# Kernel tuning notes

Measured on AMD Instinct MI355X. Metric: run time of the kernel, lower is better.

The kernel has to match this reference:

```python
import jax, jax.numpy as jnp
import numpy as np

B, S, H, F, E, K = 2, 2048, 1024, 4096, 8, 2


def setup_inputs() -> dict:
    key = jax.random.key(0)
    ks = jax.random.split(key, 5)
    scale = 0.02
    return {
        "hidden_states": jax.random.normal(ks[0], (B, S, H), jnp.float32),
        "gate_w": jax.random.normal(ks[1], (H, E), jnp.float32) * scale,  # nn.Linear(H,E,bias=False)
        "w1": jax.random.normal(ks[2], (E, H, F), jnp.float32) * scale,   # per-expert fc1
        "b1": jnp.zeros((E, F), jnp.float32),
        "w2": jax.random.normal(ks[3], (E, F, H), jnp.float32) * scale,   # per-expert fc2
        "b2": jnp.zeros((E, H), jnp.float32),
    }


def reference(hidden_states, gate_w, w1, b1, w2, b2):
    b, s, h = hidden_states.shape
    x = hidden_states.reshape(b * s, h)  # [T, H]
    T = x.shape[0]
    n_experts = gate_w.shape[1]

    # --- Top-K gating ---
    router_logits = x @ gate_w                      # [T, E]
    router_probs = jax.nn.softmax(router_logits, axis=-1)
    topk_probs, topk_idx = jax.lax.top_k(router_probs, K)  # [T, K]
    topk_probs = topk_probs / topk_probs.sum(axis=-1, keepdims=True)
    aux_loss = n_experts * jnp.sum(router_probs.mean(axis=0) ** 2)

    # --- Combine weights: scatter normalized top-k probs into dense [T, E] ---
    combine_w = jnp.zeros((T, n_experts), x.dtype).at[
        jnp.arange(T)[:, None], topk_idx
    ].add(topk_probs)

    # --- Expert MLPs (dense per-expert batched GEMM; zero combine weight drops unrouted) ---
    hidden = jax.nn.relu(jnp.einsum('th,ehf->etf', x, w1) + b1[:, None, :])  # [E, T, F]
    expert_out = jnp.einsum('etf,efh->eth', hidden, w2) + b2[:, None, :]     # [E, T, H]

    out = jnp.einsum('te,eth->th', combine_w, expert_out)  # weighted combine
    return out.reshape(b, s, h), aux_loss
```

## Files before the change

kernel.cpp:

```cpp
#include <hip/hip_runtime.h>
#include <hip/hip_bf16.h>
#include <cstdint>

#define AS1 __attribute__((address_space(1)))
#define AS3 __attribute__((address_space(3)))
#define SBAR() asm volatile("s_barrier" ::: "memory")

typedef __attribute__((ext_vector_type(8))) short short8x;
typedef __attribute__((ext_vector_type(4))) float f32x4;

static constexpr int T    = 4096;
static constexpr int HD   = 1024;
static constexpr int FD   = 4096;
static constexpr int NE   = 8;
static constexpr int P    = T * 2;
static constexpr int PPAD = P + 256;
static constexpr int MAXT256 = P / 256 + NE;
static constexpr int RTB  = 16;
static constexpr int RNB  = T / RTB;

struct TileDesc { int e; int start; int rows; int pad; };

__device__ __forceinline__ uint16_t f2bf(float f) {
  uint32_t u = __builtin_bit_cast(uint32_t, f);
  u += 0x7FFFu + ((u >> 16) & 1u);
  return (uint16_t)(u >> 16);
}
__device__ __forceinline__ float bf2f(uint16_t b) {
  uint32_t u = ((uint32_t)b) << 16;
  return __builtin_bit_cast(float, u);
}

__device__ __forceinline__ void gload_lds16(const void* g, void* l) {
  __builtin_amdgcn_global_load_lds((const AS1 uint32_t*)g, (AS3 uint32_t*)l, 16, 0, 0);
}

__device__ __forceinline__ short8x ds128(uint32_t addr) {
  short8x r;
  asm volatile("ds_read_b128 %0, %1" : "=v"(r) : "v"(addr));
  return r;
}

__global__ __launch_bounds__(256) void cvt_x_kernel(const float* __restrict__ x,
                                                    uint16_t* __restrict__ xb) {
  size_t i = ((size_t)blockIdx.x * 256 + threadIdx.x) * 4;
  float4 v = *(const float4*)&x[i];
  ushort4 o;
  o.x = f2bf(v.x); o.y = f2bf(v.y); o.z = f2bf(v.z); o.w = f2bf(v.w);
  *(ushort4*)&xb[i] = o;
}

__global__ __launch_bounds__(256) void transpose_cvt_kernel(
    const float* __restrict__ in, uint16_t* __restrict__ out, int R, int C) {
  __shared__ float tile[64][65];
  int z = blockIdx.z;
  const float* inp = in + (size_t)z * R * C;
  uint16_t* outp = out + (size_t)z * R * C;
  int r0 = blockIdx.y * 64, c0 = blockIdx.x * 64;
  int tid = threadIdx.x;
  int lr = tid >> 4;
  int lc4 = (tid & 15) * 4;
#pragma unroll
  for (int p = 0; p < 4; ++p) {
    float4 v = *(const float4*)&inp[(size_t)(r0 + lr + p * 16) * C + c0 + lc4];
    tile[lr + p * 16][lc4 + 0] = v.x;
    tile[lr + p * 16][lc4 + 1] = v.y;
    tile[lr + p * 16][lc4 + 2] = v.z;
    tile[lr + p * 16][lc4 + 3] = v.w;
  }
  __syncthreads();
#pragma unroll
  for (int p = 0; p < 4; ++p) {
    int c = lr + p * 16;
    ushort4 o;
    o.x = f2bf(tile[lc4 + 0][c]);
    o.y = f2bf(tile[lc4 + 1][c]);
    o.z = f2bf(tile[lc4 + 2][c]);
    o.w = f2bf(tile[lc4 + 3][c]);
    *(ushort4*)&outp[(size_t)(c0 + c) * R + r0 + lc4] = o;
  }
}

__global__ __launch_bounds__(256) void router_kernel(
    const float* __restrict__ x, const float* __restrict__ gate_w,
    int* __restrict__ topk_idx, float* __restrict__ topk_w,
    float* __restrict__ part_sums, int* __restrict__ part_counts) {
  __shared__ float g[NE * HD];
  __shared__ float ls[NE];
  __shared__ int   lc[NE];
  int tid = threadIdx.x;
  for (int i = tid; i < NE * HD; i += 256)
    g[(i & 7) * HD + (i >> 3)] = gate_w[i];
  if (tid < NE) { ls[tid] = 0.f; lc[tid] = 0; }
  __syncthreads();
  int wave = tid >> 6, lane = tid & 63;
  float psum[NE];
#pragma unroll
  for (int e = 0; e < NE; ++e) psum[e] = 0.f;

  for (int tt = 0; tt < RTB / 4; ++tt) {
    int t = blockIdx.x * RTB + wave * (RTB / 4) + tt;
    const float* xr = x + (size_t)t * HD;
    float acc[NE];
#pragma unroll
    for (int e = 0; e < NE; ++e) acc[e] = 0.f;
    for (int i = 0; i < HD / 64; ++i) {
      float xv = xr[lane + i * 64];
#pragma unroll
      for (int e = 0; e < NE; ++e) acc[e] += xv * g[e * HD + lane + i * 64];
    }
#pragma unroll
    for (int off = 32; off > 0; off >>= 1)
#pragma unroll
      for (int e = 0; e < NE; ++e) acc[e] += __shfl_down(acc[e], off);
    if (lane == 0) {
      float m = acc[0];
#pragma unroll
      for (int e = 1; e < NE; ++e) m = fmaxf(m, acc[e]);
      float p[NE], s = 0.f;
#pragma unroll
      for (int e = 0; e < NE; ++e) { p[e] = expf(acc[e] - m); s += p[e]; }
      float inv = 1.f / s;
#pragma unroll
      for (int e = 0; e < NE; ++e) { p[e] *= inv; psum[e] += p[e]; }
      int i0 = 0;
#pragma unroll
      for (int e = 1; e < NE; ++e) if (p[e] > p[i0]) i0 = e;
      int i1 = (i0 == 0) ? 1 : 0;
#pragma unroll
      for (int e = 0; e < NE; ++e) if (e != i0 && e != i1 && p[e] > p[i1]) i1 = e;
      float wsum = p[i0] + p[i1];
      topk_idx[t * 2] = i0; topk_idx[t * 2 + 1] = i1;
      topk_w[t * 2] = p[i0] / wsum; topk_w[t * 2 + 1] = p[i1] / wsum;
      atomicAdd(&lc[i0], 1); atomicAdd(&lc[i1], 1);
    }
  }
  if (lane == 0)
#pragma unroll
    for (int e = 0; e < NE; ++e) atomicAdd(&ls[e], psum[e]);
  __syncthreads();
  if (tid < NE) {
    part_sums[blockIdx.x * NE + tid]   = ls[tid];
    part_counts[blockIdx.x * NE + tid] = lc[tid];
  }
}

__global__ __launch_bounds__(64) void finalize_kernel(
    const int* __restrict__ part_counts, const float* __restrict__ part_sums,
    int* __restrict__ offsets, TileDesc* __restrict__ desc256,
    int* __restrict__ ntiles256, float* __restrict__ aux_out) {
  __shared__ int   csh[NE];
  __shared__ float ssh[NE];
  int tid = threadIdx.x;
  if (tid < NE) {
    int c = 0; float s = 0.f;
    for (int b = 0; b < RNB; ++b) {
      c += part_counts[b * NE + tid];
      s += part_sums[b * NE + tid];
    }
    csh[tid] = c; ssh[tid] = s;
  }
  __syncthreads();
  if (tid == 0) {
    int off = 0, nt2 = 0;
    for (int e = 0; e < NE; ++e) {
      offsets[e] = off;
      int c = csh[e];
      for (int i = 0; i < c; i += 256) {
        int rows = c - i; if (rows > 256) rows = 256;
        desc256[nt2].e = e; desc256[nt2].start = off + i; desc256[nt2].rows = rows;
        desc256[nt2].pad = 0; nt2++;
      }
      off += c;
    }
    *ntiles256 = nt2;
    float aux = 0.f;
    for (int e = 0; e < NE; ++e) {
      float mean = ssh[e] / (float)T;
      aux += mean * mean;
    }
    *aux_out = (float)NE * aux;
  }
}

__global__ __launch_bounds__(256) void scatter_kernel(
    const int* __restrict__ topk_idx, const int* __restrict__ offsets,
    int* __restrict__ fill, int* __restrict__ pair_tok, int* __restrict__ tok_pos) {
  int t = blockIdx.x * 256 + threadIdx.x;
  int lane = threadIdx.x & 63;
  unsigned long long below = (lane == 63) ? ~0ull >> 1
                                          : ((1ull << (lane + 1)) - 1) >> 1;
#pragma unroll
  for (int k = 0; k < 2; ++k) {
    int e = topk_idx[t * 2 + k];
    int pos = 0;
    for (int ex = 0; ex < NE; ++ex) {
      unsigned long long m = __ballot(e == ex);
      if (e == ex) {
        int leader = __ffsll((long long)m) - 1;
        int cnt = __popcll(m);
        int base = 0;
        if (lane == leader) base = atomicAdd(&fill[ex], cnt);
        base = __shfl(base, leader);
        pos = base + __popcll(m & below);
      }
    }
    int pp = offsets[e] + pos;
    pair_tok[pp] = t;
    tok_pos[t * 2 + k] = pp;
  }
}

template <int KD, int ND, bool GATHER, bool RELU>
__global__ __launch_bounds__(512, 2) void moe_gemm8(
    const uint16_t* __restrict__ A, const int* __restrict__ pair_tok,
    const uint16_t* __restrict__ Bw, const float* __restrict__ bias,
    uint16_t* __restrict__ C, const TileDesc* __restrict__ desc,
    const int* __restrict__ nt_ptr) {
  constexpr int NBC   = ND / 256;
  constexpr int NT    = KD / 64;
  constexpr int ASLOT = 16384;
  constexpr int BOFF  = 2 * ASLOT;
  constexpr int GRIDT = NBC * MAXT256;

  extern __shared__ char smem[];
  uint16_t* lds = (uint16_t*)smem;
  int* rowA = (int*)(smem + 131072);

  int orig = blockIdx.x;
  int work = (orig & 7) * (GRIDT / 8) + (orig >> 3);
  int nb = work % NBC;
  int mt = work / NBC;
  if (mt >= *nt_ptr) return;
  TileDesc d = desc[mt];

  int tid = threadIdx.x, lane = tid & 63, wave = tid >> 6;
  int wm = wave >> 2, wn = wave & 3;

  if constexpr (GATHER) {
    if (tid < 256) rowA[tid] = (tid < d.rows) ? pair_tok[d.start + tid] : 0;
    __syncthreads();
  }

  int wl8 = wave * 8 + (lane >> 3);
  int colel = (((lane & 7) ^ (lane >> 3)) << 3);
  const uint16_t* Asrc[4];
  const uint16_t* Bsrc[4];
#pragma unroll
  for (int i = 0; i < 4; ++i) {
    int r = i * 64 + wl8;
    int gr;
    if constexpr (GATHER) gr = rowA[r]; else gr = d.start + r;
    Asrc[i] = A + (size_t)gr * KD + colel;
    Bsrc[i] = Bw + ((size_t)d.e * ND + nb * 256 + r) * KD + colel;
  }

  auto stage = [&](int slot, int kt) {
    int ko = kt * 64;
#pragma unroll
    for (int i = 0; i < 4; ++i)
      gload_lds16(Asrc[i] + ko, &lds[slot * ASLOT + i * 4096 + wave * 512]);
#pragma unroll
    for (int j = 0; j < 4; ++j)
      gload_lds16(Bsrc[j] + ko, &lds[BOFF + slot * ASLOT + j * 4096 + wave * 512]);
  };

  uint32_t ldsu = (uint32_t)(uintptr_t)(AS3 char*)smem;
  int rd0 = (lane & 15) * 64 + ((((lane >> 4)) ^ (lane & 7)) << 3);
  int rd1 = (lane & 15) * 64 + ((((lane >> 4) | 4) ^ (lane & 7)) << 3);
  uint32_t aA0 = ldsu + (uint32_t)(wm * 8192 + rd0) * 2;
  uint32_t aA1 = ldsu + (uint32_t)(wm * 8192 + rd1) * 2;
  uint32_t aB0 = ldsu + (uint32_t)(BOFF + wn * 4096 + rd0) * 2;
  uint32_t aB1 = ldsu + (uint32_t)(BOFF + wn * 4096 + rd1) * 2;

  f32x4 acc[8][4];
#pragma unroll
  for (int i = 0; i < 8; ++i)
#pragma unroll
    for (int j = 0; j < 4; ++j) acc[i][j] = (f32x4){0.f, 0.f, 0.f, 0.f};

  short8x aq[4][2], bA[2][2], bB[2][2];

  stage(0, 0);
  stage(1, 1);
  asm volatile("s_waitcnt vmcnt(8)" ::: "memory");
  SBAR();

  for (int kt = 0; kt < NT; ++kt) {
    int slot = kt & 1;
    uint32_t sa = slot ? 32768u : 0u;

#pragma unroll
    for (int fm = 0; fm < 4; ++fm) {
      aq[fm][0] = ds128(aA0 + sa + fm * 2048);
      aq[fm][1] = ds128(aA1 + sa + fm * 2048);
    }
#pragma unroll
    for (int fn = 0; fn < 2; ++fn) {
      bA[fn][0] = ds128(aB0 + sa + fn * 2048);
      bA[fn][1] = ds128(aB1 + sa + fn * 2048);
    }
    SBAR();
    asm volatile("s_waitcnt lgkmcnt(0)" ::: "memory");
    __builtin_amdgcn_sched_barrier(0);
    __builtin_amdgcn_s_setprio(1);
#pragma unroll
    for (int fm = 0; fm < 4; ++fm)
#pragma unroll
      for (int fn = 0; fn < 2; ++fn) {
        acc[fm][fn] = __builtin_amdgcn_mfma_f32_16x16x32_bf16(aq[fm][0], bA[fn][0], acc[fm][fn], 0, 0, 0);
        acc[fm][fn] = __builtin_amdgcn_mfma_f32_16x16x32_bf16(aq[fm][1], bA[fn][1], acc[fm][fn], 0, 0, 0);
      }
    __builtin_amdgcn_s_setprio(0);
    SBAR();

#pragma unroll
    for (int fn = 0; fn < 2; ++fn) {
      bB[fn][0] = ds128(aB0 + sa + (fn + 2) * 2048);
      bB[fn][1] = ds128(aB1 + sa + (fn + 2) * 2048);
    }
    SBAR();
    asm volatile("s_waitcnt lgkmcnt(0)" ::: "memory");
    __builtin_amdgcn_sched_barrier(0);
    __builtin_amdgcn_s_setprio(1);
#pragma unroll
    for (int fm = 0; fm < 4; ++fm)
#pragma unroll
      for (int fn = 0; fn < 2; ++fn) {
        acc[fm][fn + 2] = __builtin_amdgcn_mfma_f32_16x16x32_bf16(aq[fm][0], bB[fn][0], acc[fm][fn + 2], 0, 0, 0);
        acc[fm][fn + 2] = __builtin_amdgcn_mfma_f32_16x16x32_bf16(aq[fm][1], bB[fn][1], acc[fm][fn + 2], 0, 0, 0);
      }
    __builtin_amdgcn_s_setprio(0);
    SBAR();

#pragma unroll
    for (int fm = 0; fm < 4; ++fm) {
      aq[fm][0] = ds128(aA0 + sa + 8192 + fm * 2048);
      aq[fm][1] = ds128(aA1 + sa + 8192 + fm * 2048);
    }
    SBAR();
    asm volatile("s_waitcnt lgkmcnt(0)" ::: "memory");
    __builtin_amdgcn_sched_barrier(0);
    __builtin_amdgcn_s_setprio(1);
#pragma unroll
    for (int fm = 0; fm < 4; ++fm)
#pragma unroll
      for (int fn = 0; fn < 2; ++fn) {
        acc[fm + 4][fn + 2] = __builtin_amdgcn_mfma_f32_16x16x32_bf16(aq[fm][0], bB[fn][0], acc[fm + 4][fn + 2], 0, 0, 0);
        acc[fm + 4][fn + 2] = __builtin_amdgcn_mfma_f32_16x16x32_bf16(aq[fm][1], bB[fn][1], acc[fm + 4][fn + 2], 0, 0, 0);
      }
    __builtin_amdgcn_s_setprio(0);
    SBAR();

    bool more = (kt + 2 < NT);
    if (more) stage(slot, kt + 2);
    __builtin_amdgcn_s_setprio(1);
#pragma unroll
    for (int fm = 0; fm < 4; ++fm)
#pragma unroll
      for (int fn = 0; fn < 2; ++fn) {
        acc[fm + 4][fn] = __builtin_amdgcn_mfma_f32_16x16x32_bf16(aq[fm][0], bA[fn][0], acc[fm + 4][fn], 0, 0, 0);
        acc[fm + 4][fn] = __builtin_amdgcn_mfma_f32_16x16x32_bf16(aq[fm][1], bA[fn][1], acc[fm + 4][fn], 0, 0, 0);
      }
    __builtin_amdgcn_s_setprio(0);
    if (more) asm volatile("s_waitcnt vmcnt(8)" ::: "memory");
    else      asm volatile("s_waitcnt vmcnt(0)" ::: "memory");
    SBAR();
  }

  int rq = (lane >> 4) * 4, cl = lane & 15;
  float bv[4];
#pragma unroll
  for (int fn = 0; fn < 4; ++fn)
    bv[fn] = bias[d.e * ND + nb * 256 + wn * 64 + fn * 16 + cl];
#pragma unroll
  for (int fm = 0; fm < 8; ++fm) {
    int rb = wm * 128 + fm * 16 + rq;
#pragma unroll
    for (int fn = 0; fn < 4; ++fn) {
      int col = nb * 256 + wn * 64 + fn * 16 + cl;
#pragma unroll
      for (int q = 0; q < 4; ++q) {
        int r = rb + q;
        if (r < d.rows) {
          float v = acc[fm][fn][q] + bv[fn];
          if constexpr (RELU) v = fmaxf(v, 0.f);
          C[(size_t)(d.start + r) * ND + col] = f2bf(v);
        }
      }
    }
  }
}

__global__ __launch_bounds__(256) void combine_kernel(
    const uint16_t* __restrict__ po, const int* __restrict__ tok_pos,
    const float* __restrict__ topk_w, float* __restrict__ out) {
  int t = blockIdx.x;
  int c = threadIdx.x * 4;
  int p0 = tok_pos[t * 2], p1 = tok_pos[t * 2 + 1];
  float w0 = topk_w[t * 2], w1 = topk_w[t * 2 + 1];
  ushort4 a = *(const ushort4*)&po[(size_t)p0 * HD + c];
  ushort4 b = *(const ushort4*)&po[(size_t)p1 * HD + c];
  float4 o;
  o.x = w0 * bf2f(a.x) + w1 * bf2f(b.x);
  o.y = w0 * bf2f(a.y) + w1 * bf2f(b.y);
  o.z = w0 * bf2f(a.z) + w1 * bf2f(b.z);
  o.w = w0 * bf2f(a.w) + w1 * bf2f(b.w);
  *(float4*)&out[(size_t)t * HD + c] = o;
}

extern "C" void kernel_launch(void* const* d_in, const int* in_sizes, int n_in,
                              void* d_out, int out_size, void* d_ws, size_t ws_size,
                              hipStream_t stream) {
  const float* x      = (const float*)d_in[0];
  const float* gate_w = (const float*)d_in[1];
  const float* w1     = (const float*)d_in[2];
  const float* b1     = (const float*)d_in[3];
  const float* w2     = (const float*)d_in[4];
  const float* b2     = (const float*)d_in[5];
  float* out = (float*)d_out;
  (void)in_sizes; (void)n_in; (void)out_size; (void)ws_size;

  char* w = (char*)d_ws;
  size_t off = 0;
  auto alloc = [&](size_t bytes) -> void* {
    void* p = w + off;
    off = (off + bytes + 255) & ~(size_t)255;
    return p;
  };
  int*      meta      = (int*)alloc(256);
  int*      fill      = meta;
  int*      offsets   = (int*)alloc(256);
  int*      ntiles256 = offsets + 8;
  TileDesc* desc256   = (TileDesc*)alloc(sizeof(TileDesc) * 64);
  int*      topk_idx  = (int*)alloc(sizeof(int) * P);
  float*    topk_w    = (float*)alloc(sizeof(float) * P);
  int*      tok_pos   = (int*)alloc(sizeof(int) * P);
  int*      pair_tok  = (int*)alloc(sizeof(int) * PPAD);
  float*    psums     = (float*)alloc(sizeof(float) * RNB * NE);
  int*      pcounts   = (int*)alloc(sizeof(int) * RNB * NE);
  uint16_t* xb        = (uint16_t*)alloc((size_t)T * HD * 2);
  uint16_t* w1t       = (uint16_t*)alloc((size_t)NE * FD * HD * 2);
  uint16_t* w2t       = (uint16_t*)alloc((size_t)NE * HD * FD * 2);
  uint16_t* hidden    = (uint16_t*)alloc((size_t)PPAD * FD * 2);
  uint16_t* pout      = (uint16_t*)alloc((size_t)PPAD * HD * 2);

  constexpr int GLDS = 131072 + 1024;

  hipMemsetAsync(meta, 0, 256, stream);
  cvt_x_kernel<<<(T * HD) / 1024, 256, 0, stream>>>(x, xb);
  transpose_cvt_kernel<<<dim3(FD / 64, HD / 64, NE), 256, 0, stream>>>(w1, w1t, HD, FD);
  transpose_cvt_kernel<<<dim3(HD / 64, FD / 64, NE), 256, 0, stream>>>(w2, w2t, FD, HD);
  router_kernel<<<RNB, 256, 0, stream>>>(x, gate_w, topk_idx, topk_w, psums, pcounts);
  finalize_kernel<<<1, 64, 0, stream>>>(pcounts, psums, offsets, desc256, ntiles256,
                                        out + (size_t)T * HD);
  scatter_kernel<<<T / 256, 256, 0, stream>>>(topk_idx, offsets, fill, pair_tok, tok_pos);
  moe_gemm8<HD, FD, true, true><<<(FD / 256) * MAXT256, 512, GLDS, stream>>>(
      xb, pair_tok, w1t, b1, hidden, desc256, ntiles256);
  moe_gemm8<FD, HD, false, false><<<(HD / 256) * MAXT256, 512, GLDS, stream>>>(
      hidden, nullptr, w2t, b2, pout, desc256, ntiles256);
  combine_kernel<<<T, 256, 0, stream>>>(pout, tok_pos, topk_w, out);
}
```

Before: 417.2 us.

## Use 128-row tiles for second expert GEMM and pipeline LDS reads with MFMAs

The second expert GEMM (K=4096, N=1024) now runs on 128-row M tiles with its own tile descriptor list, doubling the number of workgroups so more CUs are busy on the small-N GEMM. The grid remap now groups tiles so each of eight groups owns a contiguous set of M tiles across N blocks. The inner loop replaces the full lgkmcnt(0) waits and extra barriers with staged partial waits, so MFMAs start as soon as their operands arrive from LDS. Smaller tiles give less operand reuse per load, and the new wait counts have to match the issued reads exactly.

After: 412.1 us. About the same (-1.2%).

```diff
diff --git a/kernel.cpp b/kernel.cpp
--- a/kernel.cpp
+++ b/kernel.cpp
@@ -5,6 +5,8 @@
 #define AS1 __attribute__((address_space(1)))
 #define AS3 __attribute__((address_space(3)))
 #define SBAR() asm volatile("s_barrier" ::: "memory")
+#define LGKM_SB(n) do { asm volatile("s_waitcnt lgkmcnt(" #n ")" ::: "memory"); \
+                        __builtin_amdgcn_sched_barrier(0); } while (0)
 
 typedef __attribute__((ext_vector_type(8))) short short8x;
 typedef __attribute__((ext_vector_type(4))) float f32x4;
@@ -16,6 +18,7 @@
 static constexpr int P    = T * 2;
 static constexpr int PPAD = P + 256;
 static constexpr int MAXT256 = P / 256 + NE;
+static constexpr int MAXT128 = P / 128 + NE;
 static constexpr int RTB  = 16;
 static constexpr int RNB  = T / RTB;
 
@@ -30,11 +33,9 @@
   uint32_t u = ((uint32_t)b) << 16;
   return __builtin_bit_cast(float, u);
 }
-
 __device__ __forceinline__ void gload_lds16(const void* g, void* l) {
   __builtin_amdgcn_global_load_lds((const AS1 uint32_t*)g, (AS3 uint32_t*)l, 16, 0, 0);
 }
-
 __device__ __forceinline__ short8x ds128(uint32_t addr) {
   short8x r;
   asm volatile("ds_read_b128 %0, %1" : "=v"(r) : "v"(addr));
@@ -147,8 +148,8 @@
 
 __global__ __launch_bounds__(64) void finalize_kernel(
     const int* __restrict__ part_counts, const float* __restrict__ part_sums,
-    int* __restrict__ offsets, TileDesc* __restrict__ desc256,
-    int* __restrict__ ntiles256, float* __restrict__ aux_out) {
+    int* __restrict__ offsets, TileDesc* __restrict__ desc256, TileDesc* __restrict__ desc128,
+    int* __restrict__ ntiles256, int* __restrict__ ntiles128, float* __restrict__ aux_out) {
   __shared__ int   csh[NE];
   __shared__ float ssh[NE];
   int tid = threadIdx.x;
@@ -162,18 +163,24 @@
   }
   __syncthreads();
   if (tid == 0) {
-    int off = 0, nt2 = 0;
+    int off = 0, n2 = 0, n1 = 0;
     for (int e = 0; e < NE; ++e) {
       offsets[e] = off;
       int c = csh[e];
       for (int i = 0; i < c; i += 256) {
         int rows = c - i; if (rows > 256) rows = 256;
-        desc256[nt2].e = e; desc256[nt2].start = off + i; desc256[nt2].rows = rows;
-        desc256[nt2].pad = 0; nt2++;
+        desc256[n2].e = e; desc256[n2].start = off + i; desc256[n2].rows = rows;
+        desc256[n2].pad = 0; n2++;
+      }
+      for (int i = 0; i < c; i += 128) {
+        int rows = c - i; if (rows > 128) rows = 128;
+        desc128[n1].e = e; desc128[n1].start = off + i; desc128[n1].rows = rows;
+        desc128[n1].pad = 0; n1++;
       }
       off += c;
     }
-    *ntiles256 = nt2;
+    *ntiles256 = n2;
+    *ntiles128 = n1;
     float aux = 0.f;
     for (int e = 0; e < NE; ++e) {
       float mean = ssh[e] / (float)T;
@@ -211,7 +218,7 @@
   }
 }
 
-template <int KD, int ND, bool GATHER, bool RELU>
+template <int KD, int ND, int BM, int MAXT, bool GATHER, bool RELU>
 __global__ __launch_bounds__(512, 2) void moe_gemm8(
     const uint16_t* __restrict__ A, const int* __restrict__ pair_tok,
     const uint16_t* __restrict__ Bw, const float* __restrict__ bias,
@@ -219,153 +226,176 @@
     const int* __restrict__ nt_ptr) {
   constexpr int NBC   = ND / 256;
   constexpr int NT    = KD / 64;
-  constexpr int ASLOT = 16384;
-  constexpr int BOFF  = 2 * ASLOT;
-  constexpr int GRIDT = NBC * MAXT256;
+  constexpr int MR    = BM / 32;
+  constexpr int ABYT  = BM * 128;
+  constexpr int AREL  = 2 * BM * 64;
+  constexpr int SM    = MAXT / 8;
+  constexpr int LPT   = BM / 64 + 4;
 
   extern __shared__ char smem[];
   uint16_t* lds = (uint16_t*)smem;
-  int* rowA = (int*)(smem + 131072);
+  int* rowA = (int*)(smem + AREL * 2 + 65536);
 
   int orig = blockIdx.x;
-  int work = (orig & 7) * (GRIDT / 8) + (orig >> 3);
-  int nb = work % NBC;
-  int mt = work / NBC;
-  if (mt >= *nt_ptr) return;
-  TileDesc d = desc[mt];
+  int x = orig & 7, local = orig >> 3;
+  int nb = local / SM;
+  int mtl = x * SM + local % SM;
+  if (mtl >= *nt_ptr) return;
+  TileDesc d = desc[mtl];
 
   int tid = threadIdx.x, lane = tid & 63, wave = tid >> 6;
   int wm = wave >> 2, wn = wave & 3;
 
   if constexpr (GATHER) {
-    if (tid < 256) rowA[tid] = (tid < d.rows) ? pair_tok[d.start + tid] : 0;
+    if (tid < BM) rowA[tid] = (tid < d.rows) ? pair_tok[d.start + tid] : 0;
     __syncthreads();
   }
 
   int wl8 = wave * 8 + (lane >> 3);
   int colel = (((lane & 7) ^ (lane >> 3)) << 3);
-  const uint16_t* Asrc[4];
+  const uint16_t* Asrc[BM / 64];
   const uint16_t* Bsrc[4];
 #pragma unroll
-  for (int i = 0; i < 4; ++i) {
+  for (int i = 0; i < BM / 64; ++i) {
     int r = i * 64 + wl8;
     int gr;
     if constexpr (GATHER) gr = rowA[r]; else gr = d.start + r;
     Asrc[i] = A + (size_t)gr * KD + colel;
-    Bsrc[i] = Bw + ((size_t)d.e * ND + nb * 256 + r) * KD + colel;
-  }
+  }
+#pragma unroll
+  for (int j = 0; j < 4; ++j)
+    Bsrc[j] = Bw + ((size_t)d.e * ND + nb * 256 + j * 64 + wl8) * KD + colel;
 
   auto stage = [&](int slot, int kt) {
     int ko = kt * 64;
 #pragma unroll
-    for (int i = 0; i < 4; ++i)
-      gload_lds16(Asrc[i] + ko, &lds[slot * ASLOT + i * 4096 + wave * 512]);
+    for (int i = 0; i < BM / 64; ++i)
+      gload_lds16(Asrc[i] + ko, &lds[slot * (BM * 64) + i * 4096 + wave * 512]);
 #pragma unroll
     for (int j = 0; j < 4; ++j)
-      gload_lds16(Bsrc[j] + ko, &lds[BOFF + slot * ASLOT + j * 4096 + wave * 512]);
+      gload_lds16(Bsrc[j] + ko, &lds[AREL + slot * 16384 + j * 4096 + wave * 512]);
   };
 
   uint32_t ldsu = (uint32_t)(uintptr_t)(AS3 char*)smem;
   int rd0 = (lane & 15) * 64 + ((((lane >> 4)) ^ (lane & 7)) << 3);
   int rd1 = (lane & 15) * 64 + ((((lane >> 4) | 4) ^ (lane & 7)) << 3);
-  uint32_t aA0 = ldsu + (uint32_t)(wm * 8192 + rd0) * 2;
-  uint32_t aA1 = ldsu + (uint32_t)(wm * 8192 + rd1) * 2;
-  uint32_t aB0 = ldsu + (uint32_t)(BOFF + wn * 4096 + rd0) * 2;
-  uint32_t aB1 = ldsu + (uint32_t)(BOFF + wn * 4096 + rd1) * 2;
-
-  f32x4 acc[8][4];
-#pragma unroll
-  for (int i = 0; i < 8; ++i)
+  uint32_t aA0 = ldsu + (uint32_t)(wm * (BM * 32) + rd0) * 2;
+  uint32_t aA1 = ldsu + (uint32_t)(wm * (BM * 32) + rd1) * 2;
+  uint32_t aB0 = ldsu + (uint32_t)(AREL + wn * 4096 + rd0) * 2;
+  uint32_t aB1 = ldsu + (uint32_t)(AREL + wn * 4096 + rd1) * 2;
+
+  f32x4 acc[MR][4];
+#pragma unroll
+  for (int i = 0; i < MR; ++i)
 #pragma unroll
     for (int j = 0; j < 4; ++j) acc[i][j] = (f32x4){0.f, 0.f, 0.f, 0.f};
 
   short8x aq[4][2], bA[2][2], bB[2][2];
+  auto MM = [&](f32x4& c, const short8x& a0, const short8x& b0,
+                const short8x& a1, const short8x& b1) {
+    c = __builtin_amdgcn_mfma_f32_16x16x32_bf16(a0, b0, c, 0, 0, 0);
+    c = __builtin_amdgcn_mfma_f32_16x16x32_bf16(a1, b1, c, 0, 0, 0);
+  };
 
   stage(0, 0);
   stage(1, 1);
-  asm volatile("s_waitcnt vmcnt(8)" ::: "memory");
+  if constexpr (BM == 256) asm volatile("s_waitcnt vmcnt(8)" ::: "memory");
+  else                     asm volatile("s_waitcnt vmcnt(6)" ::: "memory");
   SBAR();
 
   for (int kt = 0; kt < NT; ++kt) {
     int slot = kt & 1;
-    uint32_t sa = slot ? 32768u : 0u;
-
+    uint32_t saA = (uint32_t)slot * ABYT;
+    uint32_t saB = (uint32_t)slot * 32768u;
+    bool more = (kt + 2 < NT);
+
+#pragma unroll
+    for (int fn = 0; fn < 2; ++fn) {
+      bA[fn][0] = ds128(aB0 + saB + fn * 2048);
+      bA[fn][1] = ds128(aB1 + saB + fn * 2048);
+    }
 #pragma unroll
     for (int fm = 0; fm < 4; ++fm) {
-      aq[fm][0] = ds128(aA0 + sa + fm * 2048);
-      aq[fm][1] = ds128(aA1 + sa + fm * 2048);
-    }
+      aq[fm][0] = ds128(aA0 + saA + fm * 2048);
+      aq[fm][1] = ds128(aA1 + saA + fm * 2048);
+    }
+    __builtin_amdgcn_s_setprio(1);
+    LGKM_SB(6);
+    MM(acc[0][0], aq[0][0], bA[0][0], aq[0][1], bA[0][1]);
+    MM(acc[0][1], aq[0][0], bA[1][0], aq[0][1], bA[1][1]);
+    LGKM_SB(4);
+    MM(acc[1][0], aq[1][0], bA[0][0], aq[1][1], bA[0][1]);
+    MM(acc[1][1], aq[1][0], bA[1][0], aq[1][1], bA[1][1]);
+    LGKM_SB(2);
+    MM(acc[2][0], aq[2][0], bA[0][0], aq[2][1], bA[0][1]);
+    MM(acc[2][1], aq[2][0], bA[1][0], aq[2][1], bA[1][1]);
+    LGKM_SB(0);
+    MM(acc[3][0], aq[3][0], bA[0][0], aq[3][1], bA[0][1]);
+    MM(acc[3][1], aq[3][0], bA[1][0], aq[3][1], bA[1][1]);
+    __builtin_amdgcn_s_setprio(0);
+
 #pragma unroll
     for (int fn = 0; fn < 2; ++fn) {
-      bA[fn][0] = ds128(aB0 + sa + fn * 2048);
-      bA[fn][1] = ds128(aB1 + sa + fn * 2048);
-    }
-    SBAR();
-    asm volatile("s_waitcnt lgkmcnt(0)" ::: "memory");
-    __builtin_amdgcn_sched_barrier(0);
+      bB[fn][0] = ds128(aB0 + saB + (fn + 2) * 2048);
+      bB[fn][1] = ds128(aB1 + saB + (fn + 2) * 2048);
+    }
     __builtin_amdgcn_s_setprio(1);
+    LGKM_SB(2);
 #pragma unroll
     for (int fm = 0; fm < 4; ++fm)
-#pragma unroll
-      for (int fn = 0; fn < 2; ++fn) {
-        acc[fm][fn] = __builtin_amdgcn_mfma_f32_16x16x32_bf16(aq[fm][0], bA[fn][0], acc[fm][fn], 0, 0, 0);
-        acc[fm][fn] = __builtin_amdgcn_mfma_f32_16x16x32_bf16(aq[fm][1], bA[fn][1], acc[fm][fn], 0, 0, 0);
-      }
-    __builtin_amdgcn_s_setprio(0);
-    SBAR();
-
-#pragma unroll
-    for (int fn = 0; fn < 2; ++fn) {
-      bB[fn][0] = ds128(aB0 + sa + (fn + 2) * 2048);
-      bB[fn][1] = ds128(aB1 + sa + (fn + 2) * 2048);
-    }
-    SBAR();
-    asm volatile("s_waitcnt lgkmcnt(0)" ::: "memory");
-    __builtin_amdgcn_sched_barrier(0);
-    __builtin_amdgcn_s_setprio(1);
-#pragma unroll
-    for (int fm = 0; fm < 4; ++fm)
-#pragma unroll
-      for (int fn = 0; fn < 2; ++fn) {
-        acc[fm][fn + 2] = __builtin_amdgcn_mfma_f32_16x16x32_bf16(aq[fm][0], bB[fn][0], acc[fm][fn + 2], 0, 0, 0);
-        acc[fm][fn + 2] = __builtin_amdgcn_mfma_f32_16x16x32_bf16(aq[fm][1], bB[fn][1], acc[fm][fn + 2], 0, 0, 0);
-      }
-    __builtin_amdgcn_s_setprio(0);
-    SBAR();
-
-#pragma unroll
-    for (int fm = 0; fm < 4; ++fm) {
-      aq[fm][0] = ds128(aA0 + sa + 8192 + fm * 2048);
-      aq[fm][1] = ds128(aA1 + sa + 8192 + fm * 2048);
-    }
-    SBAR();
-    asm volatile("s_waitcnt lgkmcnt(0)" ::: "memory");
-    __builtin_amdgcn_sched_barrier(0);
-    __builtin_amdgcn_s_setprio(1);
-#pragma unroll
-    for (int fm = 0; fm < 4; ++fm)
-#pragma unroll
-      for (int fn = 0; fn < 2; ++fn) {
-        acc[fm + 4][fn + 2] = __builtin_amdgcn_mfma_f32_16x16x32_bf16(aq[fm][0], bB[fn][0], acc[fm + 4][fn + 2], 0, 0, 0);
-        acc[fm + 4][fn + 2] = __builtin_amdgcn_mfma_f32_16x16x32_bf16(aq[fm][1], bB[fn][1], acc[fm + 4][fn + 2], 0, 0, 0);
-      }
-    __builtin_amdgcn_s_setprio(0);
-    SBAR();
-
-    bool more = (kt + 2 < NT);
-    if (more) stage(slot, kt + 2);
-    __builtin_amdgcn_s_setprio(1);
-#pragma unroll
-    for (int fm = 0; fm < 4; ++fm)
-#pragma unroll
-      for (int fn = 0; fn < 2; ++fn) {
-        acc[fm + 4][fn] = __builtin_amdgcn_mfma_f32_16x16x32_bf16(aq[fm][0], bA[fn][0], acc[fm + 4][fn], 0, 0, 0);
-        acc[fm + 4][fn] = __builtin_amdgcn_mfma_f32_16x16x32_bf16(aq[fm][1], bA[fn][1], acc[fm + 4][fn], 0, 0, 0);
-      }
-    __builtin_amdgcn_s_setprio(0);
-    if (more) asm volatile("s_waitcnt vmcnt(8)" ::: "memory");
-    else      asm volatile("s_waitcnt vmcnt(0)" ::: "memory");
-    SBAR();
+      MM(acc[fm][2], aq[fm][0], bB[0][0], aq[fm][1], bB[0][1]);
+    LGKM_SB(0);
+    if constexpr (BM == 256) {
+#pragma unroll
+      for (int fm = 0; fm < 4; ++fm)
+        MM(acc[fm][3], aq[fm][0], bB[1][0], aq[fm][1], bB[1][1]);
+      __builtin_amdgcn_s_setprio(0);
+
+#pragma unroll
+      for (int fm = 0; fm < 4; ++fm) {
+        aq[fm][0] = ds128(aA0 + saA + 8192 + fm * 2048);
+        aq[fm][1] = ds128(aA1 + saA + 8192 + fm * 2048);
+      }
+      __builtin_amdgcn_s_setprio(1);
+      LGKM_SB(6);
+      MM(acc[4][2], aq[0][0], bB[0][0], aq[0][1], bB[0][1]);
+      MM(acc[4][3], aq[0][0], bB[1][0], aq[0][1], bB[1][1]);
+      LGKM_SB(4);
+      MM(acc[5][2], aq[1][0], bB[0][0], aq[1][1], bB[0][1]);
+      MM(acc[5][3], aq[1][0], bB[1][0], aq[1][1], bB[1][1]);
+      LGKM_SB(2);
+      MM(acc[6][2], aq[2][0], bB[0][0], aq[2][1], bB[0][1]);
+      MM(acc[6][3], aq[2][0], bB[1][0], aq[2][1], bB[1][1]);
+      LGKM_SB(0);
+      MM(acc[7][2], aq[3][0], bB[0][0], aq[3][1], bB[0][1]);
+      MM(acc[7][3], aq[3][0], bB[1][0], aq[3][1], bB[1][1]);
+      __builtin_amdgcn_s_setprio(0);
+      SBAR();
+
+      if (more) stage(slot, kt + 2);
+      __builtin_amdgcn_s_setprio(1);
+#pragma unroll
+      for (int fm = 0; fm < 4; ++fm) {
+        MM(acc[fm + 4][0], aq[fm][0], bA[0][0], aq[fm][1], bA[0][1]);
+        MM(acc[fm + 4][1], aq[fm][0], bA[1][0], aq[fm][1], bA[1][1]);
+      }
+      __builtin_amdgcn_s_setprio(0);
+      if (more) asm volatile("s_waitcnt vmcnt(8)" ::: "memory");
+      else      asm volatile("s_waitcnt vmcnt(0)" ::: "memory");
+      SBAR();
+    } else {
+      __builtin_amdgcn_s_setprio(0);
+      SBAR();
+      if (more) stage(slot, kt + 2);
+      __builtin_amdgcn_s_setprio(1);
+#pragma unroll
+      for (int fm = 0; fm < 4; ++fm)
+        MM(acc[fm][3], aq[fm][0], bB[1][0], aq[fm][1], bB[1][1]);
+      __builtin_amdgcn_s_setprio(0);
+      if (more) asm volatile("s_waitcnt vmcnt(6)" ::: "memory");
+      else      asm volatile("s_waitcnt vmcnt(0)" ::: "memory");
+      SBAR();
+    }
   }
 
   int rq = (lane >> 4) * 4, cl = lane & 15;
@@ -374,8 +404,8 @@
   for (int fn = 0; fn < 4; ++fn)
     bv[fn] = bias[d.e * ND + nb * 256 + wn * 64 + fn * 16 + cl];
 #pragma unroll
-  for (int fm = 0; fm < 8; ++fm) {
-    int rb = wm * 128 + fm * 16 + rq;
+  for (int fm = 0; fm < MR; ++fm) {
+    int rb = wm * (BM / 2) + fm * 16 + rq;
 #pragma unroll
     for (int fn = 0; fn < 4; ++fn) {
       int col = nb * 256 + wn * 64 + fn * 16 + cl;
@@ -432,7 +462,9 @@
   int*      fill      = meta;
   int*      offsets   = (int*)alloc(256);
   int*      ntiles256 = offsets + 8;
+  int*      ntiles128 = offsets + 9;
   TileDesc* desc256   = (TileDesc*)alloc(sizeof(TileDesc) * 64);
+  TileDesc* desc128   = (TileDesc*)alloc(sizeof(TileDesc) * 128);
   int*      topk_idx  = (int*)alloc(sizeof(int) * P);
   float*    topk_w    = (float*)alloc(sizeof(float) * P);
   int*      tok_pos   = (int*)alloc(sizeof(int) * P);
@@ -445,19 +477,19 @@
   uint16_t* hidden    = (uint16_t*)alloc((size_t)PPAD * FD * 2);
   uint16_t* pout      = (uint16_t*)alloc((size_t)PPAD * HD * 2);
 
-  constexpr int GLDS = 131072 + 1024;
-
   hipMemsetAsync(meta, 0, 256, stream);
   cvt_x_kernel<<<(T * HD) / 1024, 256, 0, stream>>>(x, xb);
   transpose_cvt_kernel<<<dim3(FD / 64, HD / 64, NE), 256, 0, stream>>>(w1, w1t, HD, FD);
   transpose_cvt_kernel<<<dim3(HD / 64, FD / 64, NE), 256, 0, stream>>>(w2, w2t, FD, HD);
   router_kernel<<<RNB, 256, 0, stream>>>(x, gate_w, topk_idx, topk_w, psums, pcounts);
-  finalize_kernel<<<1, 64, 0, stream>>>(pcounts, psums, offsets, desc256, ntiles256,
-                                        out + (size_t)T * HD);
+  finalize_kernel<<<1, 64, 0, stream>>>(pcounts, psums, offsets, desc256, desc128,
+                                        ntiles256, ntiles128, out + (size_t)T * HD);
   scatter_kernel<<<T / 256, 256, 0, stream>>>(topk_idx, offsets, fill, pair_tok, tok_pos);
-  moe_gemm8<HD, FD, true, true><<<(FD / 256) * MAXT256, 512, GLDS, stream>>>(
+  moe_gemm8<HD, FD, 256, MAXT256, true, true>
+      <<<(FD / 256) * MAXT256, 512, 132096, stream>>>(
       xb, pair_tok, w1t, b1, hidden, desc256, ntiles256);
-  moe_gemm8<FD, HD, false, false><<<(HD / 256) * MAXT256, 512, GLDS, stream>>>(
-      hidden, nullptr, w2t, b2, pout, desc256, ntiles256);
+  moe_gemm8<FD, HD, 128, MAXT128, false, false>
+      <<<(HD / 256) * MAXT128, 512, 98304, stream>>>(
+      hidden, nullptr, w2t, b2, pout, desc128, ntiles128);
   combine_kernel<<<T, 256, 0, stream>>>(pout, tok_pos, topk_w, out);
 }
```

## Interleave MoE GEMM prefetch loads across compute phases and narrow second GEMM tile

Applied to the files above, without the earlier changes.

The global-to-LDS prefetch for the next k-tiles is split into small groups issued between the four MFMA phases, instead of one burst after the third phase. The second (down-projection) GEMM now uses a 128-wide N tile, which doubles its block count and lowers its LDS use. Block-to-tile mapping changes so that each XCD gets a contiguous range of M tiles and all N blocks of those tiles, aiming for better weight reuse in L2. LDS reads switch from inline asm to plain pointer loads, and the different vmcnt wait counts add scheduling complexity and risk.

Result: faster. 406.6 us (-2.6%).

```diff
diff --git a/kernel.cpp b/kernel.cpp
--- a/kernel.cpp
+++ b/kernel.cpp
@@ -5,6 +5,7 @@
 #define AS1 __attribute__((address_space(1)))
 #define AS3 __attribute__((address_space(3)))
 #define SBAR() asm volatile("s_barrier" ::: "memory")
+#define LGKM0() asm volatile("s_waitcnt lgkmcnt(0)" ::: "memory")
 
 typedef __attribute__((ext_vector_type(8))) short short8x;
 typedef __attribute__((ext_vector_type(4))) float f32x4;
@@ -30,15 +31,8 @@
   uint32_t u = ((uint32_t)b) << 16;
   return __builtin_bit_cast(float, u);
 }
-
 __device__ __forceinline__ void gload_lds16(const void* g, void* l) {
   __builtin_amdgcn_global_load_lds((const AS1 uint32_t*)g, (AS3 uint32_t*)l, 16, 0, 0);
-}
-
-__device__ __forceinline__ short8x ds128(uint32_t addr) {
-  short8x r;
-  asm volatile("ds_read_b128 %0, %1" : "=v"(r) : "v"(addr));
-  return r;
 }
 
 __global__ __launch_bounds__(256) void cvt_x_kernel(const float* __restrict__ x,
@@ -162,18 +156,18 @@
   }
   __syncthreads();
   if (tid == 0) {
-    int off = 0, nt2 = 0;
+    int off = 0, n2 = 0;
     for (int e = 0; e < NE; ++e) {
       offsets[e] = off;
       int c = csh[e];
       for (int i = 0; i < c; i += 256) {
         int rows = c - i; if (rows > 256) rows = 256;
-        desc256[nt2].e = e; desc256[nt2].start = off + i; desc256[nt2].rows = rows;
-        desc256[nt2].pad = 0; nt2++;
+        desc256[n2].e = e; desc256[n2].start = off + i; desc256[n2].rows = rows;
+        desc256[n2].pad = 0; n2++;
       }
       off += c;
     }
-    *ntiles256 = nt2;
+    *ntiles256 = n2;
     float aux = 0.f;
     for (int e = 0; e < NE; ++e) {
       float mean = ssh[e] / (float)T;
@@ -211,31 +205,39 @@
   }
 }
 
-template <int KD, int ND, bool GATHER, bool RELU>
+template <int KD, int ND, int BN, bool GATHER, bool RELU>
 __global__ __launch_bounds__(512, 2) void moe_gemm8(
     const uint16_t* __restrict__ A, const int* __restrict__ pair_tok,
     const uint16_t* __restrict__ Bw, const float* __restrict__ bias,
     uint16_t* __restrict__ C, const TileDesc* __restrict__ desc,
     const int* __restrict__ nt_ptr) {
-  constexpr int NBC   = ND / 256;
-  constexpr int NT    = KD / 64;
-  constexpr int ASLOT = 16384;
-  constexpr int BOFF  = 2 * ASLOT;
+  constexpr int NBC = ND / BN;
+  constexpr int NT  = KD / 64;
+  constexpr int ASL = 16384;
+  constexpr int BSL = BN * 64;
+  constexpr int BOFF = 2 * ASL;
+  constexpr int WN  = BN / 4;
+  constexpr int FN  = BN / 64;
+  constexpr int FH  = FN / 2;
+  constexpr int NGB = BN / 64;
+  constexpr int G   = 4 + NGB;
   constexpr int GRIDT = NBC * MAXT256;
+  constexpr int SMX = MAXT256 / 8;
 
   extern __shared__ char smem[];
   uint16_t* lds = (uint16_t*)smem;
-  int* rowA = (int*)(smem + 131072);
+  int* rowA = (int*)(smem + (2 * ASL + 2 * BSL) * 2);
 
   int orig = blockIdx.x;
-  int work = (orig & 7) * (GRIDT / 8) + (orig >> 3);
-  int nb = work % NBC;
-  int mt = work / NBC;
-  if (mt >= *nt_ptr) return;
-  TileDesc d = desc[mt];
+  int xcd = orig & 7, local = orig >> 3;
+  int nb = local / SMX;
+  int mtl = xcd * SMX + local % SMX;
+  if (mtl >= *nt_ptr) return;
+  TileDesc d = desc[mtl];
 
   int tid = threadIdx.x, lane = tid & 63, wave = tid >> 6;
   int wm = wave >> 2, wn = wave & 3;
+  int l15 = lane & 15, l7 = lane & 7, lk = lane >> 4;
 
   if constexpr (GATHER) {
     if (tid < 256) rowA[tid] = (tid < d.rows) ? pair_tok[d.start + tid] : 0;
@@ -245,140 +247,159 @@
   int wl8 = wave * 8 + (lane >> 3);
   int colel = (((lane & 7) ^ (lane >> 3)) << 3);
   const uint16_t* Asrc[4];
-  const uint16_t* Bsrc[4];
+  const uint16_t* Bsrc[NGB];
 #pragma unroll
   for (int i = 0; i < 4; ++i) {
     int r = i * 64 + wl8;
     int gr;
     if constexpr (GATHER) gr = rowA[r]; else gr = d.start + r;
     Asrc[i] = A + (size_t)gr * KD + colel;
-    Bsrc[i] = Bw + ((size_t)d.e * ND + nb * 256 + r) * KD + colel;
-  }
-
-  auto stage = [&](int slot, int kt) {
-    int ko = kt * 64;
-#pragma unroll
-    for (int i = 0; i < 4; ++i)
-      gload_lds16(Asrc[i] + ko, &lds[slot * ASLOT + i * 4096 + wave * 512]);
-#pragma unroll
-    for (int j = 0; j < 4; ++j)
-      gload_lds16(Bsrc[j] + ko, &lds[BOFF + slot * ASLOT + j * 4096 + wave * 512]);
+  }
+#pragma unroll
+  for (int j = 0; j < NGB; ++j)
+    Bsrc[j] = Bw + ((size_t)d.e * ND + nb * BN + j * 64 + wl8) * KD + colel;
+
+  auto stageA = [&](int tile, int i) {
+    gload_lds16(Asrc[i] + tile * 64, lds + (tile & 1) * ASL + i * 4096 + wave * 512);
   };
-
-  uint32_t ldsu = (uint32_t)(uintptr_t)(AS3 char*)smem;
-  int rd0 = (lane & 15) * 64 + ((((lane >> 4)) ^ (lane & 7)) << 3);
-  int rd1 = (lane & 15) * 64 + ((((lane >> 4) | 4) ^ (lane & 7)) << 3);
-  uint32_t aA0 = ldsu + (uint32_t)(wm * 8192 + rd0) * 2;
-  uint32_t aA1 = ldsu + (uint32_t)(wm * 8192 + rd1) * 2;
-  uint32_t aB0 = ldsu + (uint32_t)(BOFF + wn * 4096 + rd0) * 2;
-  uint32_t aB1 = ldsu + (uint32_t)(BOFF + wn * 4096 + rd1) * 2;
-
-  f32x4 acc[8][4];
+  auto stageB = [&](int tile, int j) {
+    gload_lds16(Bsrc[j] + tile * 64, lds + BOFF + (tile & 1) * BSL + j * 4096 + wave * 512);
+  };
+  auto stage_g = [&](int tile, int g) {
+    if (tile >= NT) return;
+    if constexpr (BN == 256) {
+      switch (g) {
+        case 0: stageA(tile, 0); break;
+        case 1: stageA(tile, 2); break;
+        case 2: stageB(tile, 0); break;
+        case 3: stageB(tile, 1); break;
+        case 4: stageB(tile, 2); break;
+        case 5: stageB(tile, 3); break;
+        case 6: stageA(tile, 1); break;
+        case 7: stageA(tile, 3); break;
+      }
+    } else {
+      switch (g) {
+        case 0: stageA(tile, 0); break;
+        case 1: stageA(tile, 2); break;
+        case 2: stageB(tile, 0); break;
+        case 3: stageB(tile, 1); break;
+        case 4: stageA(tile, 1); break;
+        case 5: stageA(tile, 3); break;
+      }
+    }
+  };
+
+  int aBase = (wm * 128 + l15) * 64;
+  int bBase = (wn * WN + l15) * 64;
+  int sw0 = ((lk) ^ l7) * 8;
+  int sw1 = ((4 + lk) ^ l7) * 8;
+  auto LD = [&](int o) { return *(const short8x*)(lds + o); };
+
+  f32x4 acc[8][FN];
 #pragma unroll
   for (int i = 0; i < 8; ++i)
 #pragma unroll
-    for (int j = 0; j < 4; ++j) acc[i][j] = (f32x4){0.f, 0.f, 0.f, 0.f};
-
-  short8x aq[4][2], bA[2][2], bB[2][2];
-
-  stage(0, 0);
-  stage(1, 1);
-  asm volatile("s_waitcnt vmcnt(8)" ::: "memory");
+    for (int j = 0; j < FN; ++j) acc[i][j] = (f32x4){0.f, 0.f, 0.f, 0.f};
+
+  short8x aq[4][2], bq0[FH][2], bq1[FH][2];
+  auto MM2 = [&](f32x4& c, const short8x (&a)[2], const short8x (&b)[2]) {
+    c = __builtin_amdgcn_mfma_f32_16x16x32_bf16(a[0], b[0], c, 0, 0, 0);
+    c = __builtin_amdgcn_mfma_f32_16x16x32_bf16(a[1], b[1], c, 0, 0, 0);
+  };
+
+#pragma unroll
+  for (int g = 0; g < G; ++g) stage_g(0, g);
+#pragma unroll
+  for (int g = 0; g < G - 2; ++g) stage_g(1, g);
+  if constexpr (BN == 256) asm volatile("s_waitcnt vmcnt(6)" ::: "memory");
+  else                     asm volatile("s_waitcnt vmcnt(4)" ::: "memory");
   SBAR();
 
   for (int kt = 0; kt < NT; ++kt) {
-    int slot = kt & 1;
-    uint32_t sa = slot ? 32768u : 0u;
+    const int sA = (kt & 1) * ASL;
+    const int sB = BOFF + (kt & 1) * BSL;
 
 #pragma unroll
     for (int fm = 0; fm < 4; ++fm) {
-      aq[fm][0] = ds128(aA0 + sa + fm * 2048);
-      aq[fm][1] = ds128(aA1 + sa + fm * 2048);
-    }
-#pragma unroll
-    for (int fn = 0; fn < 2; ++fn) {
-      bA[fn][0] = ds128(aB0 + sa + fn * 2048);
-      bA[fn][1] = ds128(aB1 + sa + fn * 2048);
-    }
-    SBAR();
-    asm volatile("s_waitcnt lgkmcnt(0)" ::: "memory");
-    __builtin_amdgcn_sched_barrier(0);
+      aq[fm][0] = LD(sA + aBase + fm * 1024 + sw0);
+      aq[fm][1] = LD(sA + aBase + fm * 1024 + sw1);
+    }
+#pragma unroll
+    for (int fn = 0; fn < FH; ++fn) {
+      bq0[fn][0] = LD(sB + bBase + fn * 1024 + sw0);
+      bq0[fn][1] = LD(sB + bBase + fn * 1024 + sw1);
+    }
+    stage_g(kt + 1, G - 2); stage_g(kt + 1, G - 1);
+    SBAR();
+    LGKM0();
     __builtin_amdgcn_s_setprio(1);
 #pragma unroll
     for (int fm = 0; fm < 4; ++fm)
 #pragma unroll
-      for (int fn = 0; fn < 2; ++fn) {
-        acc[fm][fn] = __builtin_amdgcn_mfma_f32_16x16x32_bf16(aq[fm][0], bA[fn][0], acc[fm][fn], 0, 0, 0);
-        acc[fm][fn] = __builtin_amdgcn_mfma_f32_16x16x32_bf16(aq[fm][1], bA[fn][1], acc[fm][fn], 0, 0, 0);
-      }
+      for (int fn = 0; fn < FH; ++fn) MM2(acc[fm][fn], aq[fm], bq0[fn]);
     __builtin_amdgcn_s_setprio(0);
     SBAR();
 
 #pragma unroll
-    for (int fn = 0; fn < 2; ++fn) {
-      bB[fn][0] = ds128(aB0 + sa + (fn + 2) * 2048);
-      bB[fn][1] = ds128(aB1 + sa + (fn + 2) * 2048);
-    }
-    SBAR();
-    asm volatile("s_waitcnt lgkmcnt(0)" ::: "memory");
-    __builtin_amdgcn_sched_barrier(0);
+    for (int fn = 0; fn < FH; ++fn) {
+      bq1[fn][0] = LD(sB + bBase + (FH + fn) * 1024 + sw0);
+      bq1[fn][1] = LD(sB + bBase + (FH + fn) * 1024 + sw1);
+    }
+    stage_g(kt + 2, 0); stage_g(kt + 2, 1);
+    SBAR();
+    LGKM0();
     __builtin_amdgcn_s_setprio(1);
 #pragma unroll
     for (int fm = 0; fm < 4; ++fm)
 #pragma unroll
-      for (int fn = 0; fn < 2; ++fn) {
-        acc[fm][fn + 2] = __builtin_amdgcn_mfma_f32_16x16x32_bf16(aq[fm][0], bB[fn][0], acc[fm][fn + 2], 0, 0, 0);
-        acc[fm][fn + 2] = __builtin_amdgcn_mfma_f32_16x16x32_bf16(aq[fm][1], bB[fn][1], acc[fm][fn + 2], 0, 0, 0);
-      }
+      for (int fn = 0; fn < FH; ++fn) MM2(acc[fm][FH + fn], aq[fm], bq1[fn]);
     __builtin_amdgcn_s_setprio(0);
     SBAR();
 
 #pragma unroll
     for (int fm = 0; fm < 4; ++fm) {
-      aq[fm][0] = ds128(aA0 + sa + 8192 + fm * 2048);
-      aq[fm][1] = ds128(aA1 + sa + 8192 + fm * 2048);
-    }
-    SBAR();
-    asm volatile("s_waitcnt lgkmcnt(0)" ::: "memory");
-    __builtin_amdgcn_sched_barrier(0);
+      aq[fm][0] = LD(sA + aBase + 4096 + fm * 1024 + sw0);
+      aq[fm][1] = LD(sA + aBase + 4096 + fm * 1024 + sw1);
+    }
+    stage_g(kt + 2, 2); stage_g(kt + 2, 3);
+    SBAR();
+    LGKM0();
     __builtin_amdgcn_s_setprio(1);
 #pragma unroll
     for (int fm = 0; fm < 4; ++fm)
 #pragma unroll
-      for (int fn = 0; fn < 2; ++fn) {
-        acc[fm + 4][fn + 2] = __builtin_amdgcn_mfma_f32_16x16x32_bf16(aq[fm][0], bB[fn][0], acc[fm + 4][fn + 2], 0, 0, 0);
-        acc[fm + 4][fn + 2] = __builtin_amdgcn_mfma_f32_16x16x32_bf16(aq[fm][1], bB[fn][1], acc[fm + 4][fn + 2], 0, 0, 0);
-      }
+      for (int fn = 0; fn < FH; ++fn) MM2(acc[4 + fm][FH + fn], aq[fm], bq1[fn]);
     __builtin_amdgcn_s_setprio(0);
     SBAR();
 
-    bool more = (kt + 2 < NT);
-    if (more) stage(slot, kt + 2);
+    if constexpr (BN == 256) { stage_g(kt + 2, 4); stage_g(kt + 2, 5); }
     __builtin_amdgcn_s_setprio(1);
 #pragma unroll
     for (int fm = 0; fm < 4; ++fm)
 #pragma unroll
-      for (int fn = 0; fn < 2; ++fn) {
-        acc[fm + 4][fn] = __builtin_amdgcn_mfma_f32_16x16x32_bf16(aq[fm][0], bA[fn][0], acc[fm + 4][fn], 0, 0, 0);
-        acc[fm + 4][fn] = __builtin_amdgcn_mfma_f32_16x16x32_bf16(aq[fm][1], bA[fn][1], acc[fm + 4][fn], 0, 0, 0);
-      }
+      for (int fn = 0; fn < FH; ++fn) MM2(acc[4 + fm][fn], aq[fm], bq0[fn]);
     __builtin_amdgcn_s_setprio(0);
-    if (more) asm volatile("s_waitcnt vmcnt(8)" ::: "memory");
-    else      asm volatile("s_waitcnt vmcnt(0)" ::: "memory");
-    SBAR();
-  }
-
-  int rq = (lane >> 4) * 4, cl = lane & 15;
-  float bv[4];
-#pragma unroll
-  for (int fn = 0; fn < 4; ++fn)
-    bv[fn] = bias[d.e * ND + nb * 256 + wn * 64 + fn * 16 + cl];
+    if (kt + 2 < NT) {
+      if constexpr (BN == 256) asm volatile("s_waitcnt vmcnt(6)" ::: "memory");
+      else                     asm volatile("s_waitcnt vmcnt(4)" ::: "memory");
+    } else {
+      asm volatile("s_waitcnt vmcnt(0)" ::: "memory");
+    }
+    SBAR();
+  }
+
+  int rq = lk * 4, cl = l15;
+  float bv[FN];
+#pragma unroll
+  for (int fn = 0; fn < FN; ++fn)
+    bv[fn] = bias[d.e * ND + nb * BN + wn * WN + fn * 16 + cl];
 #pragma unroll
   for (int fm = 0; fm < 8; ++fm) {
-    int rb = wm * 128 + fm * 16 + rq;
-#pragma unroll
-    for (int fn = 0; fn < 4; ++fn) {
-      int col = nb * 256 + wn * 64 + fn * 16 + cl;
+    int rb = wm * 128 + (fm & 3) * 16 + (fm >> 2) * 64 + rq;
+#pragma unroll
+    for (int fn = 0; fn < FN; ++fn) {
+      int col = nb * BN + wn * WN + fn * 16 + cl;
 #pragma unroll
       for (int q = 0; q < 4; ++q) {
         int r = rb + q;
@@ -445,8 +466,6 @@
   uint16_t* hidden    = (uint16_t*)alloc((size_t)PPAD * FD * 2);
   uint16_t* pout      = (uint16_t*)alloc((size_t)PPAD * HD * 2);
 
-  constexpr int GLDS = 131072 + 1024;
-
   hipMemsetAsync(meta, 0, 256, stream);
   cvt_x_kernel<<<(T * HD) / 1024, 256, 0, stream>>>(x, xb);
   transpose_cvt_kernel<<<dim3(FD / 64, HD / 64, NE), 256, 0, stream>>>(w1, w1t, HD, FD);
@@ -455,9 +474,11 @@
   finalize_kernel<<<1, 64, 0, stream>>>(pcounts, psums, offsets, desc256, ntiles256,
                                         out + (size_t)T * HD);
   scatter_kernel<<<T / 256, 256, 0, stream>>>(topk_idx, offsets, fill, pair_tok, tok_pos);
-  moe_gemm8<HD, FD, true, true><<<(FD / 256) * MAXT256, 512, GLDS, stream>>>(
+  moe_gemm8<HD, FD, 256, true, true>
+      <<<(FD / 256) * MAXT256, 512, 132096, stream>>>(
       xb, pair_tok, w1t, b1, hidden, desc256, ntiles256);
-  moe_gemm8<FD, HD, false, false><<<(HD / 256) * MAXT256, 512, GLDS, stream>>>(
+  moe_gemm8<FD, HD, 128, false, false>
+      <<<(HD / 128) * MAXT256, 512, 98304, stream>>>(
       hidden, nullptr, w2t, b2, pout, desc256, ntiles256);
   combine_kernel<<<T, 256, 0, stream>>>(pout, tok_pos, topk_w, out);
 }
```
